# Performance work log

Measured on AMD Instinct MI355X. Metric: run time of the kernel, lower is better.

The kernel has to match this reference:

```python
import jax, jax.numpy as jnp
import numpy as np
from jax import lax

N = 4096
D = 256          # dim_hidden
DU = 1024        # dim_uni
G = 2000         # num_genes
E = 4            # num_experts
K = 1            # top-k
H = 4            # attention heads
HD = D // H      # head dim = 64
MAP = 64         # fourier mapping_size


def _ln(x, g, b, eps=1e-5):
    m = jnp.mean(x, axis=-1, keepdims=True)
    v = jnp.var(x, axis=-1, keepdims=True)
    return (x - m) * lax.rsqrt(v + eps) * g + b


def setup_inputs() -> dict:
    key = jax.random.key(0)
    ks = jax.random.split(key, 32)
    s = 0.02
    inp = {
        "vis": jax.random.normal(ks[0], (N, DU), jnp.float32),
        "pos": jax.random.uniform(ks[1], (N, 3), jnp.float32),
        "grad": jax.random.uniform(ks[2], (N, 1), jnp.float32),
        # FourierEncoding buffer: randn(3, 64) * scale(10)
        "B_fourier": jax.random.normal(ks[3], (3, MAP), jnp.float32) * 10.0,
        # img_enc
        "W_img": jax.random.normal(ks[4], (DU, D), jnp.float32) * s,
        "b_img": jnp.zeros((D,), jnp.float32),
        # pos_enc linear: Linear(128, 256)
        "W_pos": jax.random.normal(ks[5], (2 * MAP, D), jnp.float32) * s,
        "b_pos": jnp.zeros((D,), jnp.float32),
        # MultiheadAttention projections
        "Wq": jax.random.normal(ks[6], (D, D), jnp.float32) * s,
        "bq": jnp.zeros((D,), jnp.float32),
        "Wk": jax.random.normal(ks[7], (D, D), jnp.float32) * s,
        "bk": jnp.zeros((D,), jnp.float32),
        "Wv": jax.random.normal(ks[8], (D, D), jnp.float32) * s,
        "bv": jnp.zeros((D,), jnp.float32),
        "Wo": jax.random.normal(ks[9], (D, D), jnp.float32) * s,
        "bo": jnp.zeros((D,), jnp.float32),
        "ln1_g": jnp.ones((D,), jnp.float32),
        "ln1_b": jnp.zeros((D,), jnp.float32),
        # MoE router: Linear(D+1, E)
        "W_router": jax.random.normal(ks[10], (D + 1, E), jnp.float32) * s,
        "b_router": jnp.zeros((E,), jnp.float32),
        # experts: stacked [E, ...] FFN weights
        "W1e": jax.random.normal(ks[11], (E, D, 4 * D), jnp.float32) * s,
        "b1e": jnp.zeros((E, 4 * D), jnp.float32),
        "W2e": jax.random.normal(ks[12], (E, 4 * D, D), jnp.float32) * s,
        "b2e": jnp.zeros((E, D), jnp.float32),
        # gene decoder
        "Wg1": jax.random.normal(ks[13], (D, D), jnp.float32) * s,
        "bg1": jnp.zeros((D,), jnp.float32),
        "lng_g": jnp.ones((D,), jnp.float32),
        "lng_b": jnp.zeros((D,), jnp.float32),
        "Wg2": jax.random.normal(ks[14], (D, 2 * G), jnp.float32) * s,
        "bg2": jnp.zeros((2 * G,), jnp.float32),
        # func head
        "Wf1": jax.random.normal(ks[15], (D, 64), jnp.float32) * s,
        "bf1": jnp.zeros((64,), jnp.float32),
        "Wf2": jax.random.normal(ks[16], (64, 1), jnp.float32) * s,
        "bf2": jnp.zeros((1,), jnp.float32),
    }
    return inp


def reference(vis, pos, grad, B_fourier, W_img, b_img, W_pos, b_pos,
              Wq, bq, Wk, bk, Wv, bv, Wo, bo, ln1_g, ln1_b,
              W_router, b_router, W1e, b1e, W2e, b2e,
              Wg1, bg1, lng_g, lng_b, Wg2, bg2, Wf1, bf1, Wf2, bf2):
    # --- encoders ---
    x_proj = (2.0 * np.pi) * (pos @ B_fourier)                 # [N, 64]
    fourier = jnp.concatenate([jnp.sin(x_proj), jnp.cos(x_proj)], axis=-1)  # [N,128]
    z = vis @ W_img + b_img + fourier @ W_pos + b_pos          # [N, D]

    # --- spatial context attention (batch=1 full self-attention) ---
    q = (z @ Wq + bq).reshape(N, H, HD)
    k = (z @ Wk + bk).reshape(N, H, HD)
    v = (z @ Wv + bv).reshape(N, H, HD)
    scores = jnp.einsum('nhd,mhd->hnm', q, k) / np.sqrt(HD)    # [H, N, N]
    attn = jax.nn.softmax(scores, axis=-1)
    ctx = jnp.einsum('hnm,mhd->nhd', attn, v).reshape(N, D)
    attn_out = ctx @ Wo + bo
    z = _ln(z + attn_out, ln1_g, ln1_b)

    # --- sparse MoE (top-1 routing, gated dense expert combine) ---
    router_in = jnp.concatenate([z, grad], axis=-1)            # [N, D+1]
    logits = router_in @ W_router + b_router                   # [N, E]
    probs = jax.nn.softmax(logits, axis=-1)
    topk_p, topk_i = lax.top_k(probs, K)                       # [N, K]
    gate = jnp.sum(jax.nn.one_hot(topk_i, E, dtype=z.dtype) * topk_p[..., None], axis=1)  # [N, E]
    h = jax.nn.gelu(jnp.einsum('nd,edf->nef', z, W1e) + b1e, approximate=False)  # [N,E,4D]
    y = jnp.einsum('nef,efd->ned', h, W2e) + b2e               # [N, E, D]
    z = z + jnp.einsum('ne,ned->nd', gate, y)

    # --- gene decoder ---
    d = jax.nn.gelu(_ln(z @ Wg1 + bg1, lng_g, lng_b), approximate=False)
    preds = (d @ Wg2 + bg2).reshape(N, G, 2)
    mu = jax.nn.softplus(preds[:, :, 0])
    theta = jax.nn.softplus(preds[:, :, 1]) + 1e-6

    # --- functional head ---
    g = jax.nn.sigmoid(jax.nn.gelu(z @ Wf1 + bf1, approximate=False) @ Wf2 + bf2)
    return mu, theta, g
```

## Files before the change

kernel.cpp:

```cpp
#include <hip/hip_runtime.h>
#include <math.h>

#define NTOK 4096
#define DMODEL 256
#define G_GENES 2000

typedef _Float16 f16;
typedef _Float16 f16x8 __attribute__((ext_vector_type(8)));
typedef float f32x4 __attribute__((ext_vector_type(4)));

__device__ __forceinline__ float gelu_exact(float x) {
    return 0.5f * x * (1.0f + erff(x * 0.70710678118654752f));
}
__device__ __forceinline__ float softplus_fast(float x) {
    return fmaxf(x, 0.0f) + __logf(1.0f + __expf(-fabsf(x)));
}

__global__ __launch_bounds__(256) void encin_k(const float* __restrict__ vis,
                                               const float* __restrict__ pos,
                                               const float* __restrict__ B,
                                               f16* __restrict__ Abig) {
    int n = blockIdx.x, t = threadIdx.x;
    float4 v = *(const float4*)(vis + (size_t)n * 1024 + t * 4);
    union { ushort4 u; f16 h[4]; } o;
    o.h[0] = (f16)v.x; o.h[1] = (f16)v.y; o.h[2] = (f16)v.z; o.h[3] = (f16)v.w;
    *(ushort4*)(Abig + (size_t)n * 1152 + t * 4) = o.u;
    if (t < 64) {
        float xp = 6.283185307179586f *
                   (pos[n * 3 + 0] * B[t] + pos[n * 3 + 1] * B[64 + t] + pos[n * 3 + 2] * B[128 + t]);
        Abig[(size_t)n * 1152 + 1024 + t] = (f16)sinf(xp);
        Abig[(size_t)n * 1152 + 1088 + t] = (f16)cosf(xp);
    }
}

struct TD { const float* s; f16* d; int R, C; int ldo; };
struct TDs { TD t[17]; int pre[18]; };
__global__ __launch_bounds__(256) void tconv_k(TDs ds) {
    int bid = blockIdx.x;
    int ti = 0;
#pragma unroll
    for (int i = 0; i < 17; i++)
        if (bid >= ds.pre[i + 1]) ti = i + 1;
    TD td = ds.t[ti];
    int local = bid - ds.pre[ti];
    int yt = td.C >> 5;
    int r0 = (local / yt) << 5;
    int c0 = (local % yt) << 5;
    __shared__ float tile[32][33];
    int tx = threadIdx.x & 31, ty = threadIdx.x >> 5;
#pragma unroll
    for (int i = 0; i < 32; i += 8)
        tile[ty + i][tx] = td.s[(size_t)(r0 + ty + i) * td.C + c0 + tx];
    __syncthreads();
#pragma unroll
    for (int i = 0; i < 32; i += 8)
        td.d[(size_t)(c0 + ty + i) * td.ldo + r0 + tx] = (f16)tile[tx][ty + i];
}

__global__ __launch_bounds__(256) void tconvh_k(const f16* __restrict__ src, int ldin,
                                                f16* __restrict__ dst, int ldo) {
    __shared__ f16 tile[32][33];
    int r0 = blockIdx.x * 32, c0 = blockIdx.y * 32;
    int tx = threadIdx.x & 31, ty = threadIdx.x >> 5;
#pragma unroll
    for (int i = 0; i < 32; i += 8)
        tile[ty + i][tx] = src[(size_t)(r0 + ty + i) * ldin + c0 + tx];
    __syncthreads();
#pragma unroll
    for (int i = 0; i < 32; i += 8)
        dst[(size_t)(c0 + ty + i) * ldo + r0 + tx] = tile[tx][ty + i];
}

__global__ __launch_bounds__(256) void setup_k(const float* b_img, const float* b_pos,
                                               const float* bq, const float* bk, const float* bv,
                                               const float* bg1, const float* bf1,
                                               float* benc, float* biasqkv, float* bgf) {
    int t = threadIdx.x;
    benc[t] = b_img[t] + b_pos[t];
    biasqkv[t] = bq[t];
    biasqkv[256 + t] = bk[t];
    biasqkv[512 + t] = bv[t];
    bgf[t] = bg1[t];
    if (t < 64) bgf[256 + t] = bf1[t];
}

#define EPI_F32 0
#define EPI_DUAL 1
#define EPI_F16 2
#define EPI_GELU_F16 3
#define EPI_GENE 4
#define EPI_MOESC 5
#define EPI_GF 6

template <int MTN, int EPI, int MODE>
__global__ __launch_bounds__(256) void bgemm_k(
    const f16* __restrict__ A, int lda,
    const f16* __restrict__ B, int ldb,
    const float* __restrict__ bias,
    float* __restrict__ Cf, f16* __restrict__ Ch, int ldc,
    int Ncols, int K,
    size_t eB, size_t eBias,
    const int* __restrict__ gidx, const int* __restrict__ temap,
    const float* __restrict__ z2, const float* __restrict__ gval,
    float* __restrict__ outMu, float* __restrict__ outTheta) {
    constexpr int BN = MTN * 32;
    __shared__ __align__(16) char smem[(128 + BN) * 72 * 2];
    f16 (*As)[72] = (f16(*)[72])smem;
    f16 (*Bs)[72] = (f16(*)[72])(smem + (size_t)128 * 72 * 2);

    const int tid = threadIdx.x;
    const int m0 = blockIdx.x * 128;
    const int n0 = blockIdx.y * BN;
    const int w = tid >> 6, lane = tid & 63;
    const int wr = w >> 1, wc = w & 1;
    const int ln = lane & 15, lg = lane >> 4;
    const int sr = tid >> 3;
    const int sc = (tid & 7) * 8;

    if (MODE == 1 || MODE == 2) {
        int e = temap[blockIdx.x];
        B += (size_t)e * eB;
        if (bias) bias += (size_t)e * eBias;
    }

    int grows[4];
#pragma unroll
    for (int i = 0; i < 4; i++) {
        int r = m0 + sr + i * 32;
        if (MODE == 1) {
            int g = gidx[r];
            grows[i] = (g < 0) ? 0 : g;
        } else {
            grows[i] = r;
        }
    }

    f32x4 acc[4][MTN];
    f32x4 zf = {0.f, 0.f, 0.f, 0.f};
#pragma unroll
    for (int i = 0; i < 4; i++)
#pragma unroll
        for (int j = 0; j < MTN; j++) acc[i][j] = zf;

    for (int k0 = 0; k0 < K; k0 += 64) {
#pragma unroll
        for (int i = 0; i < 4; i++) {
            uint4 v = *(const uint4*)(A + (size_t)grows[i] * lda + k0 + sc);
            int r = sr + i * 32;
            *(uint2*)&As[r][sc] = make_uint2(v.x, v.y);
            *(uint2*)&As[r][sc + 4] = make_uint2(v.z, v.w);
        }
#pragma unroll
        for (int i = 0; i < MTN; i++) {
            int r = sr + i * 32;
            uint4 v = make_uint4(0, 0, 0, 0);
            if (n0 + r < Ncols) v = *(const uint4*)(B + (size_t)(n0 + r) * ldb + k0 + sc);
            *(uint2*)&Bs[r][sc] = make_uint2(v.x, v.y);
            *(uint2*)&Bs[r][sc + 4] = make_uint2(v.z, v.w);
        }
        __syncthreads();
#pragma unroll
        for (int ks = 0; ks < 64; ks += 32) {
            f16x8 a[4], b[MTN];
#pragma unroll
            for (int t = 0; t < 4; t++) {
                const f16* p = &As[wr * 64 + t * 16 + ln][ks + lg * 8];
                union { f16x8 f; uint2 u[2]; } tmp;
                tmp.u[0] = *(const uint2*)p;
                tmp.u[1] = *(const uint2*)(p + 4);
                a[t] = tmp.f;
            }
#pragma unroll
            for (int t = 0; t < MTN; t++) {
                const f16* p = &Bs[wc * (MTN * 16) + t * 16 + ln][ks + lg * 8];
                union { f16x8 f; uint2 u[2]; } tmp;
                tmp.u[0] = *(const uint2*)p;
                tmp.u[1] = *(const uint2*)(p + 4);
                b[t] = tmp.f;
            }
#pragma unroll
            for (int tm = 0; tm < 4; tm++)
#pragma unroll
                for (int tn = 0; tn < MTN; tn++)
                    acc[tm][tn] = __builtin_amdgcn_mfma_f32_16x16x32_f16(a[tm], b[tn], acc[tm][tn], 0, 0, 0);
        }
        __syncthreads();
    }

    if (EPI == EPI_GENE) {
        float bval[MTN];
#pragma unroll
        for (int tn = 0; tn < MTN; tn++) {
            int col = n0 + wc * (MTN * 16) + tn * 16 + ln;
            bval[tn] = (col < Ncols) ? bias[col] : 0.0f;
        }
        float* Cs = (float*)smem;
        const int rrow = tid >> 3;
        const int rseg = tid & 7;
#pragma unroll
        for (int tm = 0; tm < 4; tm++) {
            __syncthreads();
#pragma unroll
            for (int tn = 0; tn < MTN; tn++) {
                int lc = wc * (MTN * 16) + tn * 16 + ln;
#pragma unroll
                for (int i = 0; i < 4; i++) {
                    int lr = wr * 16 + lg * 4 + i;
                    Cs[lr * 132 + lc] = acc[tm][tn][i] + bval[tn];
                }
            }
            __syncthreads();
            int grow = m0 + ((rrow >> 4) * 64) + tm * 16 + (rrow & 15);
            const float* cr = &Cs[rrow * 132 + rseg * 16];
            float mu[8], th[8];
#pragma unroll
            for (int g = 0; g < 8; g++) {
                mu[g] = softplus_fast(cr[2 * g]);
                th[g] = softplus_fast(cr[2 * g + 1]) + 1e-6f;
            }
            int gbase = (n0 + rseg * 16) >> 1;
            float* mp = outMu + (size_t)grow * G_GENES + gbase;
            float* tp = outTheta + (size_t)grow * G_GENES + gbase;
            if (gbase + 8 <= G_GENES) {
                *(float4*)mp = make_float4(mu[0], mu[1], mu[2], mu[3]);
                *(float4*)(mp + 4) = make_float4(mu[4], mu[5], mu[6], mu[7]);
                *(float4*)tp = make_float4(th[0], th[1], th[2], th[3]);
                *(float4*)(tp + 4) = make_float4(th[4], th[5], th[6], th[7]);
            } else {
#pragma unroll
                for (int g = 0; g < 8; g++)
                    if (gbase + g < G_GENES) { mp[g] = mu[g]; tp[g] = th[g]; }
            }
        }
        return;
    }

#pragma unroll
    for (int tm = 0; tm < 4; tm++) {
#pragma unroll
        for (int tn = 0; tn < MTN; tn++) {
            int col = n0 + wc * (MTN * 16) + tn * 16 + ln;
            if (col >= Ncols) continue;
#pragma unroll
            for (int i = 0; i < 4; i++) {
                int row = m0 + wr * 64 + tm * 16 + lg * 4 + i;
                float v = acc[tm][tn][i];
                if (EPI == EPI_MOESC) {
                    int tok = gidx[row];
                    if (tok < 0) continue;
                    v += bias[col];
                    size_t oi = (size_t)tok * ldc + col;
                    Ch[oi] = (f16)(z2[oi] + gval[tok] * v);
                    continue;
                }
                if (EPI == EPI_GF) {
                    v += bias[col];
                    if (col < 256) Cf[(size_t)row * 256 + col] = v;
                    else Ch[(size_t)row * 64 + (col - 256)] = (f16)gelu_exact(v);
                    continue;
                }
                size_t idx = (size_t)row * ldc + col;
                if (EPI == EPI_F32) {
                    if (bias) v += bias[col];
                    Cf[idx] = v;
                } else if (EPI == EPI_DUAL) {
                    v += bias[col];
                    Cf[idx] = v;
                    Ch[idx] = (f16)v;
                } else if (EPI == EPI_F16) {
                    v += bias[col];
                    Ch[idx] = (f16)v;
                } else if (EPI == EPI_GELU_F16) {
                    v += bias[col];
                    Ch[idx] = (f16)gelu_exact(v);
                }
            }
        }
    }
}

__global__ __launch_bounds__(256) void flash_k(const f16* __restrict__ qkv,
                                               const f16* __restrict__ Vt,
                                               f16* __restrict__ Opart16,
                                               float2* __restrict__ mlpart) {
    __shared__ f16 Ks[64][72];
    __shared__ f16 Vts[64][72];
    __shared__ f16 Ps[4][16][72];
    const int tid = threadIdx.x;
    const int w = tid >> 6, lane = tid & 63;
    const int ln = lane & 15, quad = lane >> 4;
    const int q0 = blockIdx.x * 64;
    const int hq = blockIdx.y * 64;
    const int kt0 = blockIdx.z * 8;

    f16x8 qfrag[2];
    {
        const f16* qp = qkv + (size_t)(q0 + w * 16 + ln) * 768 + hq + quad * 8;
        union { f16x8 f; uint4 u; } t0, t1;
        t0.u = *(const uint4*)qp;
        t1.u = *(const uint4*)(qp + 32);
        qfrag[0] = t0.f; qfrag[1] = t1.f;
    }

    const int srow = tid >> 2;
    const int scol = (tid & 3) * 16;

    float m_run[4], l_run[4];
    f32x4 Oacc[4];
#pragma unroll
    for (int i = 0; i < 4; i++) {
        m_run[i] = -1e30f; l_run[i] = 0.0f;
        Oacc[i] = (f32x4){0.f, 0.f, 0.f, 0.f};
    }

    uint4 kreg[2], vreg[2];
    {
        const f16* kp = qkv + (size_t)(kt0 * 64 + srow) * 768 + 256 + hq + scol;
        const f16* vp = Vt + (size_t)(hq + srow) * 4096 + kt0 * 64 + scol;
        kreg[0] = *(const uint4*)kp; kreg[1] = *(const uint4*)(kp + 8);
        vreg[0] = *(const uint4*)vp; vreg[1] = *(const uint4*)(vp + 8);
    }

    for (int kt = kt0; kt < kt0 + 8; kt++) {
        __syncthreads();
        *(uint4*)&Ks[srow][scol] = kreg[0];
        *(uint4*)&Ks[srow][scol + 8] = kreg[1];
        *(uint4*)&Vts[srow][scol] = vreg[0];
        *(uint4*)&Vts[srow][scol + 8] = vreg[1];
        __syncthreads();
        if (kt + 1 < kt0 + 8) {
            const f16* kp = qkv + (size_t)((kt + 1) * 64 + srow) * 768 + 256 + hq + scol;
            const f16* vp = Vt + (size_t)(hq + srow) * 4096 + (kt + 1) * 64 + scol;
            kreg[0] = *(const uint4*)kp; kreg[1] = *(const uint4*)(kp + 8);
            vreg[0] = *(const uint4*)vp; vreg[1] = *(const uint4*)(vp + 8);
        }

        f32x4 accS[4];
#pragma unroll
        for (int nt = 0; nt < 4; nt++) {
            union { f16x8 f; uint4 u; } b0, b1;
            b0.u = *(const uint4*)&Ks[nt * 16 + ln][quad * 8];
            b1.u = *(const uint4*)&Ks[nt * 16 + ln][32 + quad * 8];
            f32x4 a = {0.f, 0.f, 0.f, 0.f};
            a = __builtin_amdgcn_mfma_f32_16x16x32_f16(qfrag[0], b0.f, a, 0, 0, 0);
            a = __builtin_amdgcn_mfma_f32_16x16x32_f16(qfrag[1], b1.f, a, 0, 0, 0);
            accS[nt] = a;
        }
#pragma unroll
        for (int nt = 0; nt < 4; nt++)
#pragma unroll
            for (int i = 0; i < 4; i++) accS[nt][i] *= 0.125f;

        float mnew[4], alpha[4], rs[4];
#pragma unroll
        for (int i = 0; i < 4; i++) {
            float mx = fmaxf(fmaxf(accS[0][i], accS[1][i]), fmaxf(accS[2][i], accS[3][i]));
            mx = fmaxf(mx, __shfl_xor(mx, 1));
            mx = fmaxf(mx, __shfl_xor(mx, 2));
            mx = fmaxf(mx, __shfl_xor(mx, 4));
            mx = fmaxf(mx, __shfl_xor(mx, 8));
            mnew[i] = fmaxf(m_run[i], mx);
            rs[i] = 0.0f;
        }
#pragma unroll
        for (int nt = 0; nt < 4; nt++)
#pragma unroll
            for (int i = 0; i < 4; i++) {
                float p = __expf(accS[nt][i] - mnew[i]);
                accS[nt][i] = p;
                rs[i] += p;
            }
#pragma unroll
        for (int i = 0; i < 4; i++) {
            float s = rs[i];
            s += __shfl_xor(s, 1);
            s += __shfl_xor(s, 2);
            s += __shfl_xor(s, 4);
            s += __shfl_xor(s, 8);
            alpha[i] = __expf(m_run[i] - mnew[i]);
            l_run[i] = l_run[i] * alpha[i] + s;
            m_run[i] = mnew[i];
        }
#pragma unroll
        for (int dt = 0; dt < 4; dt++)
#pragma unroll
            for (int i = 0; i < 4; i++) Oacc[dt][i] *= alpha[i];

#pragma unroll
        for (int nt = 0; nt < 4; nt++)
#pragma unroll
            for (int i = 0; i < 4; i++)
                Ps[w][quad * 4 + i][nt * 16 + ln] = (f16)accS[nt][i];

        union { f16x8 f; uint4 u; } pf0, pf1;
        pf0.u = *(const uint4*)&Ps[w][ln][quad * 8];
        pf1.u = *(const uint4*)&Ps[w][ln][32 + quad * 8];
#pragma unroll
        for (int dt = 0; dt < 4; dt++) {
            union { f16x8 f; uint4 u; } b0, b1;
            b0.u = *(const uint4*)&Vts[dt * 16 + ln][quad * 8];
            b1.u = *(const uint4*)&Vts[dt * 16 + ln][32 + quad * 8];
            Oacc[dt] = __builtin_amdgcn_mfma_f32_16x16x32_f16(pf0.f, b0.f, Oacc[dt], 0, 0, 0);
            Oacc[dt] = __builtin_amdgcn_mfma_f32_16x16x32_f16(pf1.f, b1.f, Oacc[dt], 0, 0, 0);
        }
    }

    const int slot = blockIdx.x * 4 + blockIdx.y;
    f16* op = Opart16 + ((((size_t)blockIdx.z * 256 + slot) * 4 + w) * 64 + lane) * 16;
    union { uint4 u; f16 h[8]; } pk0, pk1;
#pragma unroll
    for (int dt = 0; dt < 2; dt++)
#pragma unroll
        for (int i = 0; i < 4; i++) pk0.h[dt * 4 + i] = (f16)Oacc[dt][i];
#pragma unroll
    for (int dt = 2; dt < 4; dt++)
#pragma unroll
        for (int i = 0; i < 4; i++) pk1.h[(dt - 2) * 4 + i] = (f16)Oacc[dt][i];
    *(uint4*)op = pk0.u;
    *(uint4*)(op + 8) = pk1.u;
    if (ln == 0) {
#pragma unroll
        for (int i = 0; i < 4; i++)
            mlpart[(size_t)(blockIdx.z * 4 + blockIdx.y) * NTOK + q0 + w * 16 + quad * 4 + i] =
                make_float2(m_run[i], l_run[i]);
    }
}

__global__ __launch_bounds__(256) void fcomb_k(const f16* __restrict__ Opart16,
                                               const float2* __restrict__ mlpart,
                                               f16* __restrict__ ctxbf) {
    const int slot = blockIdx.x;
    const int w = threadIdx.x >> 6, lane = threadIdx.x & 63;
    const int bx = slot >> 2, h = slot & 3;
    const int quad = lane >> 4, ln = lane & 15;
    const int nbase = bx * 64 + w * 16 + quad * 4;

    float2 ml[8][4];
    float mmax[4] = {-1e30f, -1e30f, -1e30f, -1e30f};
#pragma unroll
    for (int s = 0; s < 8; s++)
#pragma unroll
        for (int i = 0; i < 4; i++) {
            ml[s][i] = mlpart[(size_t)(s * 4 + h) * NTOK + nbase + i];
            mmax[i] = fmaxf(mmax[i], ml[s][i].x);
        }
    float L[4] = {0.f, 0.f, 0.f, 0.f};
    float wgt[8][4];
#pragma unroll
    for (int s = 0; s < 8; s++)
#pragma unroll
        for (int i = 0; i < 4; i++) {
            wgt[s][i] = __expf(ml[s][i].x - mmax[i]);
            L[i] += wgt[s][i] * ml[s][i].y;
        }

    float acc[16];
#pragma unroll
    for (int j = 0; j < 16; j++) acc[j] = 0.f;
#pragma unroll
    for (int s = 0; s < 8; s++) {
        const f16* op = Opart16 + ((((size_t)s * 256 + slot) * 4 + w) * 64 + lane) * 16;
        union { uint4 u; f16 h[8]; } p0, p1;
        p0.u = *(const uint4*)op;
        p1.u = *(const uint4*)(op + 8);
#pragma unroll
        for (int dt = 0; dt < 2; dt++)
#pragma unroll
            for (int i = 0; i < 4; i++) acc[dt * 4 + i] += wgt[s][i] * (float)p0.h[dt * 4 + i];
#pragma unroll
        for (int dt = 2; dt < 4; dt++)
#pragma unroll
            for (int i = 0; i < 4; i++) acc[dt * 4 + i] += wgt[s][i] * (float)p1.h[(dt - 2) * 4 + i];
    }
    float inv[4];
#pragma unroll
    for (int i = 0; i < 4; i++) inv[i] = 1.0f / L[i];
#pragma unroll
    for (int dt = 0; dt < 4; dt++)
#pragma unroll
        for (int i = 0; i < 4; i++)
            ctxbf[(size_t)(nbase + i) * 256 + h * 64 + dt * 16 + ln] = (f16)(acc[dt * 4 + i] * inv[i]);
}

template <int DO_ROUTER>
__global__ __launch_bounds__(256) void ln_k(const float* __restrict__ X,
                                            const float* __restrict__ R,
                                            const float* __restrict__ gam,
                                            const float* __restrict__ bet,
                                            float* __restrict__ Of, f16* __restrict__ Oh, int doGelu,
                                            const float* __restrict__ grad,
                                            const float* __restrict__ Wr,
                                            const float* __restrict__ br,
                                            int* __restrict__ eid, float* __restrict__ gval) {
    __shared__ float sm[4];
    __shared__ float smr[16];
    int n = blockIdx.x, c = threadIdx.x;
    float x = X[(size_t)n * DMODEL + c];
    if (R) x += R[(size_t)n * DMODEL + c];
    float s = x;
    for (int off = 32; off; off >>= 1) s += __shfl_down(s, off);
    if ((c & 63) == 0) sm[c >> 6] = s;
    __syncthreads();
    float mean = (sm[0] + sm[1] + sm[2] + sm[3]) * (1.0f / DMODEL);
    float d = x - mean;
    float s2 = d * d;
    for (int off = 32; off; off >>= 1) s2 += __shfl_down(s2, off);
    __syncthreads();
    if ((c & 63) == 0) sm[c >> 6] = s2;
    __syncthreads();
    float var = (sm[0] + sm[1] + sm[2] + sm[3]) * (1.0f / DMODEL);
    float y = d * rsqrtf(var + 1e-5f) * gam[c] + bet[c];
    if (doGelu) y = gelu_exact(y);
    size_t idx = (size_t)n * DMODEL + c;
    if (Of) Of[idx] = y;
    if (Oh) Oh[idx] = (f16)y;

    if (DO_ROUTER) {
        float p0 = y * Wr[c * 4 + 0], p1 = y * Wr[c * 4 + 1];
        float p2 = y * Wr[c * 4 + 2], p3 = y * Wr[c * 4 + 3];
        for (int off = 32; off; off >>= 1) {
            p0 += __shfl_down(p0, off);
            p1 += __shfl_down(p1, off);
            p2 += __shfl_down(p2, off);
            p3 += __shfl_down(p3, off);
        }
        int wv = c >> 6;
        if ((c & 63) == 0) {
            smr[wv * 4 + 0] = p0; smr[wv * 4 + 1] = p1;
            smr[wv * 4 + 2] = p2; smr[wv * 4 + 3] = p3;
        }
        __syncthreads();
        if (c == 0) {
            float gv = grad[n];
            float l[4];
#pragma unroll
            for (int e = 0; e < 4; e++)
                l[e] = smr[e] + smr[4 + e] + smr[8 + e] + smr[12 + e] + gv * Wr[256 * 4 + e] + br[e];
            float mx = fmaxf(fmaxf(l[0], l[1]), fmaxf(l[2], l[3]));
            float ex[4], ssum = 0;
#pragma unroll
            for (int e = 0; e < 4; e++) { ex[e] = __expf(l[e] - mx); ssum += ex[e]; }
            int am = 0;
            float best = l[0];
#pragma unroll
            for (int e = 1; e < 4; e++)
                if (l[e] > best) { best = l[e]; am = e; }
            eid[n] = am;
            gval[n] = ex[am] / ssum;
        }
    }
}

__global__ __launch_bounds__(256) void compact_k(const int* __restrict__ eid,
                                                 int* __restrict__ gidx,
                                                 int* __restrict__ temap) {
    __shared__ int cnt[4], poff[4], cur[4];
    int t = threadIdx.x;
    if (t < 4) cnt[t] = 0;
    __syncthreads();
    for (int it = 0; it < 16; it++)
        atomicAdd(&cnt[eid[it * 256 + t]], 1);
    __syncthreads();
    if (t == 0) {
        int o = 0;
        for (int e = 0; e < 4; e++) {
            poff[e] = o;
            cur[e] = o;
            o += (cnt[e] + 127) & ~127;
        }
    }
    __syncthreads();
    if (t < 36) {
        int e = 0;
        for (int x = 0; x < 4; x++) {
            int seg0 = poff[x] >> 7;
            int seg1 = (poff[x] + ((cnt[x] + 127) & ~127)) >> 7;
            if (t >= seg0 && t < seg1) e = x;
        }
        temap[t] = e;
    }
    for (int i = t; i < 4608; i += 256) gidx[i] = -1;
    __syncthreads();
    for (int it = 0; it < 16; it++) {
        int n = it * 256 + t;
        int slot = atomicAdd(&cur[eid[n]], 1);
        gidx[slot] = n;
    }
}

__global__ __launch_bounds__(256) void ghead_k(const f16* __restrict__ f,
                                               const float* __restrict__ Wf2,
                                               const float* __restrict__ bf2,
                                               float* __restrict__ out) {
    int n = blockIdx.x * 256 + threadIdx.x;
    float s = bf2[0];
#pragma unroll
    for (int c = 0; c < 8; c++) {
        union { uint4 u; f16 h[8]; } t;
        t.u = *(const uint4*)(f + (size_t)n * 64 + c * 8);
#pragma unroll
        for (int j = 0; j < 8; j++) s = fmaf((float)t.h[j], Wf2[c * 8 + j], s);
    }
    out[n] = 1.0f / (1.0f + expf(-s));
}

extern "C" void kernel_launch(void* const* d_in, const int* in_sizes, int n_in,
                              void* d_out, int out_size, void* d_ws, size_t ws_size,
                              hipStream_t stream) {
    const float* vis   = (const float*)d_in[0];
    const float* pos   = (const float*)d_in[1];
    const float* grad  = (const float*)d_in[2];
    const float* Bf    = (const float*)d_in[3];
    const float* W_img = (const float*)d_in[4];
    const float* b_img = (const float*)d_in[5];
    const float* W_pos = (const float*)d_in[6];
    const float* b_pos = (const float*)d_in[7];
    const float* Wq = (const float*)d_in[8];  const float* bq = (const float*)d_in[9];
    const float* Wk = (const float*)d_in[10]; const float* bk = (const float*)d_in[11];
    const float* Wv = (const float*)d_in[12]; const float* bv = (const float*)d_in[13];
    const float* Wo = (const float*)d_in[14]; const float* bo = (const float*)d_in[15];
    const float* ln1g = (const float*)d_in[16]; const float* ln1b = (const float*)d_in[17];
    const float* Wr = (const float*)d_in[18]; const float* br = (const float*)d_in[19];
    const float* W1e = (const float*)d_in[20]; const float* b1e = (const float*)d_in[21];
    const float* W2e = (const float*)d_in[22]; const float* b2e = (const float*)d_in[23];
    const float* Wg1 = (const float*)d_in[24]; const float* bg1 = (const float*)d_in[25];
    const float* lngg = (const float*)d_in[26]; const float* lngb = (const float*)d_in[27];
    const float* Wg2 = (const float*)d_in[28]; const float* bg2 = (const float*)d_in[29];
    const float* Wf1 = (const float*)d_in[30]; const float* bf1 = (const float*)d_in[31];
    const float* Wf2 = (const float*)d_in[32]; const float* bf2 = (const float*)d_in[33];

    float* out = (float*)d_out;
    float* outMu = out;
    float* outTh = out + (size_t)NTOK * G_GENES;
    float* outG  = out + (size_t)2 * NTOK * G_GENES;

    char* base = (char*)d_ws;
    size_t off = 0;
    auto A8 = [&](size_t bytes) { char* p = base + off; off += (bytes + 255) & ~(size_t)255; return p; };

    char* reg1 = A8(16 * 1024 * 1024);
    f16* Abig    = (f16*)reg1;
    f16* Opart16 = (f16*)reg1;
    char* reg2 = A8(20 * 1024 * 1024);
    f16* qkvbf = (f16*)reg2;
    f16* hh    = (f16*)(reg2 + 8 * 1024 * 1024);

    f16* WtEnc = (f16*)A8((size_t)256 * 1152 * 2);
    f16* Wqkvt = (f16*)A8((size_t)768 * 256 * 2);
    f16* Wot   = (f16*)A8((size_t)256 * 256 * 2);
    f16* W1t   = (f16*)A8((size_t)4 * 1024 * 256 * 2);
    f16* W2t   = (f16*)A8((size_t)4 * 256 * 1024 * 2);
    f16* Wgft  = (f16*)A8((size_t)320 * 256 * 2);
    f16* Wg2t  = (f16*)A8((size_t)4000 * 256 * 2);
    f16* Vt    = (f16*)A8((size_t)256 * NTOK * 2);
    float2* mlpart = (float2*)A8((size_t)32 * NTOK * 8);
    float* benc    = (float*)A8(256 * 4);
    float* biasqkv = (float*)A8(768 * 4);
    float* bgf     = (float*)A8(320 * 4);
    float* z    = (float*)A8((size_t)NTOK * DMODEL * 4);
    float* z2   = (float*)A8((size_t)NTOK * DMODEL * 4);
    float* attn = (float*)A8((size_t)NTOK * DMODEL * 4);
    float* tbuf = (float*)A8((size_t)NTOK * DMODEL * 4);
    f16* zbf    = (f16*)A8((size_t)NTOK * DMODEL * 2);
    f16* z2bf   = (f16*)A8((size_t)NTOK * DMODEL * 2);
    f16* z3bf   = (f16*)A8((size_t)NTOK * DMODEL * 2);
    f16* ctxbf  = (f16*)A8((size_t)NTOK * DMODEL * 2);
    f16* dbufbf = (f16*)A8((size_t)NTOK * DMODEL * 2);
    f16* fbf    = (f16*)A8((size_t)NTOK * 64 * 2);
    int* eidb   = (int*)A8(NTOK * 4);
    float* gval = (float*)A8(NTOK * 4);
    int* gidx   = (int*)A8(4608 * 4);
    int* temap  = (int*)A8(64 * 4);

    dim3 blk(256);

    TDs td;
    int nd = 0, pre = 0;
    auto addT = [&](const float* s, f16* d, int R, int C, int ldo) {
        td.t[nd] = TD{s, d, R, C, ldo};
        td.pre[nd] = pre;
        pre += (R >> 5) * (C >> 5);
        nd++;
    };
    addT(W_img, WtEnc, 1024, 256, 1152);
    addT(W_pos, WtEnc + 1024, 128, 256, 1152);
    addT(Wq, Wqkvt, 256, 256, 256);
    addT(Wk, Wqkvt + 256 * 256, 256, 256, 256);
    addT(Wv, Wqkvt + 512 * 256, 256, 256, 256);
    addT(Wo, Wot, 256, 256, 256);
    for (int e = 0; e < 4; e++) addT(W1e + (size_t)e * 262144, W1t + (size_t)e * 262144, 256, 1024, 256);
    for (int e = 0; e < 4; e++) addT(W2e + (size_t)e * 262144, W2t + (size_t)e * 262144, 1024, 256, 1024);
    addT(Wg1, Wgft, 256, 256, 256);
    addT(Wf1, Wgft + 256 * 256, 256, 64, 256);
    addT(Wg2, Wg2t, 256, 4000, 256);
    td.pre[nd] = pre;
    tconv_k<<<pre, blk, 0, stream>>>(td);
    setup_k<<<1, blk, 0, stream>>>(b_img, b_pos, bq, bk, bv, bg1, bf1, benc, biasqkv, bgf);

    encin_k<<<NTOK, blk, 0, stream>>>(vis, pos, Bf, Abig);
    bgemm_k<1, EPI_DUAL, 0><<<dim3(32, 8, 1), blk, 0, stream>>>(
        Abig, 1152, WtEnc, 1152, benc, z, zbf, 256, 256, 1152,
        0, 0, nullptr, nullptr, nullptr, nullptr, nullptr, nullptr);

    bgemm_k<2, EPI_F16, 0><<<dim3(32, 12, 1), blk, 0, stream>>>(
        zbf, 256, Wqkvt, 256, biasqkv, nullptr, qkvbf, 768, 768, 256,
        0, 0, nullptr, nullptr, nullptr, nullptr, nullptr, nullptr);
    tconvh_k<<<dim3(128, 8, 1), blk, 0, stream>>>(qkvbf + 512, 768, Vt, 4096);

    flash_k<<<dim3(64, 4, 8), blk, 0, stream>>>(qkvbf, Vt, Opart16, mlpart);
    fcomb_k<<<256, blk, 0, stream>>>(Opart16, mlpart, ctxbf);
    bgemm_k<1, EPI_F32, 0><<<dim3(32, 8, 1), blk, 0, stream>>>(
        ctxbf, 256, Wot, 256, bo, attn, nullptr, 256, 256, 256,
        0, 0, nullptr, nullptr, nullptr, nullptr, nullptr, nullptr);
    ln_k<1><<<NTOK, blk, 0, stream>>>(z, attn, ln1g, ln1b, z2, z2bf, 0, grad, Wr, br, eidb, gval);

    compact_k<<<1, blk, 0, stream>>>(eidb, gidx, temap);
    bgemm_k<4, EPI_GELU_F16, 1><<<dim3(36, 8, 1), blk, 0, stream>>>(
        z2bf, 256, W1t, 256, b1e, nullptr, hh, 1024, 1024, 256,
        262144, 1024, gidx, temap, nullptr, nullptr, nullptr, nullptr);
    bgemm_k<2, EPI_MOESC, 2><<<dim3(36, 4, 1), blk, 0, stream>>>(
        hh, 1024, W2t, 1024, b2e, nullptr, z3bf, 256, 256, 1024,
        262144, 256, gidx, temap, z2, gval, nullptr, nullptr);

    bgemm_k<1, EPI_GF, 0><<<dim3(32, 10, 1), blk, 0, stream>>>(
        z3bf, 256, Wgft, 256, bgf, tbuf, fbf, 256, 320, 256,
        0, 0, nullptr, nullptr, nullptr, nullptr, nullptr, nullptr);
    ln_k<0><<<NTOK, blk, 0, stream>>>(tbuf, nullptr, lngg, lngb, nullptr, dbufbf, 1,
                                      nullptr, nullptr, nullptr, nullptr, nullptr);
    bgemm_k<4, EPI_GENE, 0><<<dim3(32, 32, 1), blk, 0, stream>>>(
        dbufbf, 256, Wg2t, 256, bg2, nullptr, nullptr, 4000, 4000, 256,
        0, 0, nullptr, nullptr, nullptr, nullptr, outMu, outTh);

    ghead_k<<<NTOK / 256, blk, 0, stream>>>(fbf, Wf2, bf2, outG);
}
```

Baseline: 479.2 us.

## Transpose flash attention MFMA, double-buffer K/V, halve KV splits, retile MoE down-proj

The flash-attention kernel swaps the MFMA operand order, computing S^T, so each lane holds a single query row. This turns the row max and sum into two cross-quad shuffles and lets P be rebuilt in registers via shuffles instead of a shared-memory round trip. K/V tiles are double-buffered in LDS with one barrier per tile, and each block covers 16 key tiles instead of 8, which halves the split-K partials that fcomb has to merge. fcomb now writes its output through LDS to get vectorized stores, and the MoE second GEMM changes its tile template from 2 to 1 with twice as many column blocks. Fewer splits reduce parallelism in flash_k (1024 blocks instead of 2048) in exchange for less combine traffic.

```diff
diff --git a/kernel.cpp b/kernel.cpp
--- a/kernel.cpp
+++ b/kernel.cpp
@@ -6,6 +6,7 @@
 #define G_GENES 2000
 
 typedef _Float16 f16;
+typedef _Float16 f16x2 __attribute__((ext_vector_type(2)));
 typedef _Float16 f16x8 __attribute__((ext_vector_type(8)));
 typedef float f32x4 __attribute__((ext_vector_type(4)));
 
@@ -14,6 +15,11 @@
 }
 __device__ __forceinline__ float softplus_fast(float x) {
     return fmaxf(x, 0.0f) + __logf(1.0f + __expf(-fabsf(x)));
+}
+__device__ __forceinline__ unsigned pkf16(float a, float b) {
+    union { f16x2 h; unsigned u; } t;
+    t.h = (f16x2){(f16)a, (f16)b};
+    return t.u;
 }
 
 __global__ __launch_bounds__(256) void encin_k(const float* __restrict__ vis,
@@ -283,15 +289,14 @@
                                                const f16* __restrict__ Vt,
                                                f16* __restrict__ Opart16,
                                                float2* __restrict__ mlpart) {
-    __shared__ f16 Ks[64][72];
-    __shared__ f16 Vts[64][72];
-    __shared__ f16 Ps[4][16][72];
+    __shared__ f16 Kb[2][64][72];
+    __shared__ f16 Vb[2][64][72];
     const int tid = threadIdx.x;
     const int w = tid >> 6, lane = tid & 63;
     const int ln = lane & 15, quad = lane >> 4;
     const int q0 = blockIdx.x * 64;
     const int hq = blockIdx.y * 64;
-    const int kt0 = blockIdx.z * 8;
+    const int kt0 = blockIdx.z * 16;
 
     f16x8 qfrag[2];
     {
@@ -305,104 +310,106 @@
     const int srow = tid >> 2;
     const int scol = (tid & 3) * 16;
 
-    float m_run[4], l_run[4];
-    f32x4 Oacc[4];
-#pragma unroll
-    for (int i = 0; i < 4; i++) {
-        m_run[i] = -1e30f; l_run[i] = 0.0f;
-        Oacc[i] = (f32x4){0.f, 0.f, 0.f, 0.f};
-    }
-
-    uint4 kreg[2], vreg[2];
-    {
-        const f16* kp = qkv + (size_t)(kt0 * 64 + srow) * 768 + 256 + hq + scol;
-        const f16* vp = Vt + (size_t)(hq + srow) * 4096 + kt0 * 64 + scol;
-        kreg[0] = *(const uint4*)kp; kreg[1] = *(const uint4*)(kp + 8);
-        vreg[0] = *(const uint4*)vp; vreg[1] = *(const uint4*)(vp + 8);
-    }
-
-    for (int kt = kt0; kt < kt0 + 8; kt++) {
+    float m_run = -1e30f, l_run = 0.0f;
+    f32x4 accO[4];
+#pragma unroll
+    for (int i = 0; i < 4; i++) accO[i] = (f32x4){0.f, 0.f, 0.f, 0.f};
+
+    uint4 kA[2], vA[2], kB[2], vB[2];
+    auto loadKV = [&](int kt, uint4* kr, uint4* vr) {
+        const f16* kp = qkv + (size_t)(kt * 64 + srow) * 768 + 256 + hq + scol;
+        const f16* vp = Vt + (size_t)(hq + srow) * 4096 + kt * 64 + scol;
+        kr[0] = *(const uint4*)kp; kr[1] = *(const uint4*)(kp + 8);
+        vr[0] = *(const uint4*)vp; vr[1] = *(const uint4*)(vp + 8);
+    };
+    auto stage = [&](int b, const uint4* kr, const uint4* vr) {
+        *(uint4*)&Kb[b][srow][scol] = kr[0];
+        *(uint4*)&Kb[b][srow][scol + 8] = kr[1];
+        *(uint4*)&Vb[b][srow][scol] = vr[0];
+        *(uint4*)&Vb[b][srow][scol + 8] = vr[1];
+    };
+
+    auto computeTile = [&](int b) {
+        f32x4 accS[4];
+#pragma unroll
+        for (int nt = 0; nt < 4; nt++) {
+            union { f16x8 f; uint4 u; } a0, a1;
+            a0.u = *(const uint4*)&Kb[b][nt * 16 + ln][quad * 8];
+            a1.u = *(const uint4*)&Kb[b][nt * 16 + ln][32 + quad * 8];
+            f32x4 a = {0.f, 0.f, 0.f, 0.f};
+            a = __builtin_amdgcn_mfma_f32_16x16x32_f16(a0.f, qfrag[0], a, 0, 0, 0);
+            a = __builtin_amdgcn_mfma_f32_16x16x32_f16(a1.f, qfrag[1], a, 0, 0, 0);
+            accS[nt] = a;
+        }
+        float mx = -1e30f;
+#pragma unroll
+        for (int nt = 0; nt < 4; nt++)
+#pragma unroll
+            for (int i = 0; i < 4; i++) {
+                accS[nt][i] *= 0.125f;
+                mx = fmaxf(mx, accS[nt][i]);
+            }
+        mx = fmaxf(mx, __shfl_xor(mx, 16));
+        mx = fmaxf(mx, __shfl_xor(mx, 32));
+        float mnew = fmaxf(m_run, mx);
+        float rs = 0.0f;
+#pragma unroll
+        for (int nt = 0; nt < 4; nt++)
+#pragma unroll
+            for (int i = 0; i < 4; i++) {
+                float p = __expf(accS[nt][i] - mnew);
+                accS[nt][i] = p;
+                rs += p;
+            }
+        rs += __shfl_xor(rs, 16);
+        rs += __shfl_xor(rs, 32);
+        float alpha = __expf(m_run - mnew);
+        l_run = l_run * alpha + rs;
+        m_run = mnew;
+#pragma unroll
+        for (int dt = 0; dt < 4; dt++)
+#pragma unroll
+            for (int i = 0; i < 4; i++) accO[dt][i] *= alpha;
+
+#pragma unroll
+        for (int c = 0; c < 2; c++) {
+            unsigned p0x = pkf16(accS[2 * c][0], accS[2 * c][1]);
+            unsigned p0y = pkf16(accS[2 * c][2], accS[2 * c][3]);
+            unsigned p1x = pkf16(accS[2 * c + 1][0], accS[2 * c + 1][1]);
+            unsigned p1y = pkf16(accS[2 * c + 1][2], accS[2 * c + 1][3]);
+            unsigned x16_0x = __shfl_xor((int)p0x, 16), x16_0y = __shfl_xor((int)p0y, 16);
+            unsigned x32_0x = __shfl_xor((int)p0x, 32), x32_0y = __shfl_xor((int)p0y, 32);
+            unsigned x48_0x = __shfl_xor((int)p0x, 48), x48_0y = __shfl_xor((int)p0y, 48);
+            unsigned x16_1x = __shfl_xor((int)p1x, 16), x16_1y = __shfl_xor((int)p1y, 16);
+            unsigned x32_1x = __shfl_xor((int)p1x, 32), x32_1y = __shfl_xor((int)p1y, 32);
+            unsigned x48_1x = __shfl_xor((int)p1x, 48), x48_1y = __shfl_xor((int)p1y, 48);
+            union { f16x8 f; unsigned u[4]; } pf;
+            pf.u[0] = quad == 0 ? p0x : quad == 1 ? x48_0x : quad == 2 ? x32_1x : x16_1x;
+            pf.u[1] = quad == 0 ? p0y : quad == 1 ? x48_0y : quad == 2 ? x32_1y : x16_1y;
+            pf.u[2] = quad == 0 ? x16_0x : quad == 1 ? x32_0x : quad == 2 ? x48_1x : p1x;
+            pf.u[3] = quad == 0 ? x16_0y : quad == 1 ? x32_0y : quad == 2 ? x48_1y : p1y;
+#pragma unroll
+            for (int dt = 0; dt < 4; dt++) {
+                union { f16x8 f; uint4 u; } vf;
+                vf.u = *(const uint4*)&Vb[b][dt * 16 + ln][c * 32 + quad * 8];
+                accO[dt] = __builtin_amdgcn_mfma_f32_16x16x32_f16(vf.f, pf.f, accO[dt], 0, 0, 0);
+            }
+        }
+    };
+
+    loadKV(kt0, kA, vA);
+    stage(0, kA, vA);
+    loadKV(kt0 + 1, kB, vB);
+    __syncthreads();
+    for (int t = 0; t < 16; t += 2) {
+        computeTile(0);
+        stage(1, kB, vB);
+        if (t + 2 < 16) loadKV(kt0 + t + 2, kA, vA);
         __syncthreads();
-        *(uint4*)&Ks[srow][scol] = kreg[0];
-        *(uint4*)&Ks[srow][scol + 8] = kreg[1];
-        *(uint4*)&Vts[srow][scol] = vreg[0];
-        *(uint4*)&Vts[srow][scol + 8] = vreg[1];
+        computeTile(1);
+        if (t + 2 < 16) stage(0, kA, vA);
+        if (t + 3 < 16) loadKV(kt0 + t + 3, kB, vB);
         __syncthreads();
-        if (kt + 1 < kt0 + 8) {
-            const f16* kp = qkv + (size_t)((kt + 1) * 64 + srow) * 768 + 256 + hq + scol;
-            const f16* vp = Vt + (size_t)(hq + srow) * 4096 + (kt + 1) * 64 + scol;
-            kreg[0] = *(const uint4*)kp; kreg[1] = *(const uint4*)(kp + 8);
-            vreg[0] = *(const uint4*)vp; vreg[1] = *(const uint4*)(vp + 8);
-        }
-
-        f32x4 accS[4];
-#pragma unroll
-        for (int nt = 0; nt < 4; nt++) {
-            union { f16x8 f; uint4 u; } b0, b1;
-            b0.u = *(const uint4*)&Ks[nt * 16 + ln][quad * 8];
-            b1.u = *(const uint4*)&Ks[nt * 16 + ln][32 + quad * 8];
-            f32x4 a = {0.f, 0.f, 0.f, 0.f};
-            a = __builtin_amdgcn_mfma_f32_16x16x32_f16(qfrag[0], b0.f, a, 0, 0, 0);
-            a = __builtin_amdgcn_mfma_f32_16x16x32_f16(qfrag[1], b1.f, a, 0, 0, 0);
-            accS[nt] = a;
-        }
-#pragma unroll
-        for (int nt = 0; nt < 4; nt++)
-#pragma unroll
-            for (int i = 0; i < 4; i++) accS[nt][i] *= 0.125f;
-
-        float mnew[4], alpha[4], rs[4];
-#pragma unroll
-        for (int i = 0; i < 4; i++) {
-            float mx = fmaxf(fmaxf(accS[0][i], accS[1][i]), fmaxf(accS[2][i], accS[3][i]));
-            mx = fmaxf(mx, __shfl_xor(mx, 1));
-            mx = fmaxf(mx, __shfl_xor(mx, 2));
-            mx = fmaxf(mx, __shfl_xor(mx, 4));
-            mx = fmaxf(mx, __shfl_xor(mx, 8));
-            mnew[i] = fmaxf(m_run[i], mx);
-            rs[i] = 0.0f;
-        }
-#pragma unroll
-        for (int nt = 0; nt < 4; nt++)
-#pragma unroll
-            for (int i = 0; i < 4; i++) {
-                float p = __expf(accS[nt][i] - mnew[i]);
-                accS[nt][i] = p;
-                rs[i] += p;
-            }
-#pragma unroll
-        for (int i = 0; i < 4; i++) {
-            float s = rs[i];
-            s += __shfl_xor(s, 1);
-            s += __shfl_xor(s, 2);
-            s += __shfl_xor(s, 4);
-            s += __shfl_xor(s, 8);
-            alpha[i] = __expf(m_run[i] - mnew[i]);
-            l_run[i] = l_run[i] * alpha[i] + s;
-            m_run[i] = mnew[i];
-        }
-#pragma unroll
-        for (int dt = 0; dt < 4; dt++)
-#pragma unroll
-            for (int i = 0; i < 4; i++) Oacc[dt][i] *= alpha[i];
-
-#pragma unroll
-        for (int nt = 0; nt < 4; nt++)
-#pragma unroll
-            for (int i = 0; i < 4; i++)
-                Ps[w][quad * 4 + i][nt * 16 + ln] = (f16)accS[nt][i];
-
-        union { f16x8 f; uint4 u; } pf0, pf1;
-        pf0.u = *(const uint4*)&Ps[w][ln][quad * 8];
-        pf1.u = *(const uint4*)&Ps[w][ln][32 + quad * 8];
-#pragma unroll
-        for (int dt = 0; dt < 4; dt++) {
-            union { f16x8 f; uint4 u; } b0, b1;
-            b0.u = *(const uint4*)&Vts[dt * 16 + ln][quad * 8];
-            b1.u = *(const uint4*)&Vts[dt * 16 + ln][32 + quad * 8];
-            Oacc[dt] = __builtin_amdgcn_mfma_f32_16x16x32_f16(pf0.f, b0.f, Oacc[dt], 0, 0, 0);
-            Oacc[dt] = __builtin_amdgcn_mfma_f32_16x16x32_f16(pf1.f, b1.f, Oacc[dt], 0, 0, 0);
-        }
     }
 
     const int slot = blockIdx.x * 4 + blockIdx.y;
@@ -411,75 +418,68 @@
 #pragma unroll
     for (int dt = 0; dt < 2; dt++)
 #pragma unroll
-        for (int i = 0; i < 4; i++) pk0.h[dt * 4 + i] = (f16)Oacc[dt][i];
+        for (int i = 0; i < 4; i++) pk0.h[dt * 4 + i] = (f16)accO[dt][i];
 #pragma unroll
     for (int dt = 2; dt < 4; dt++)
 #pragma unroll
-        for (int i = 0; i < 4; i++) pk1.h[(dt - 2) * 4 + i] = (f16)Oacc[dt][i];
+        for (int i = 0; i < 4; i++) pk1.h[(dt - 2) * 4 + i] = (f16)accO[dt][i];
     *(uint4*)op = pk0.u;
     *(uint4*)(op + 8) = pk1.u;
-    if (ln == 0) {
-#pragma unroll
-        for (int i = 0; i < 4; i++)
-            mlpart[(size_t)(blockIdx.z * 4 + blockIdx.y) * NTOK + q0 + w * 16 + quad * 4 + i] =
-                make_float2(m_run[i], l_run[i]);
-    }
+    if (quad == 0)
+        mlpart[(size_t)(blockIdx.z * 4 + blockIdx.y) * NTOK + q0 + w * 16 + ln] =
+            make_float2(m_run, l_run);
 }
 
 __global__ __launch_bounds__(256) void fcomb_k(const f16* __restrict__ Opart16,
                                                const float2* __restrict__ mlpart,
                                                f16* __restrict__ ctxbf) {
+    __shared__ f16 Os[4][16][72];
     const int slot = blockIdx.x;
     const int w = threadIdx.x >> 6, lane = threadIdx.x & 63;
     const int bx = slot >> 2, h = slot & 3;
     const int quad = lane >> 4, ln = lane & 15;
-    const int nbase = bx * 64 + w * 16 + quad * 4;
-
-    float2 ml[8][4];
-    float mmax[4] = {-1e30f, -1e30f, -1e30f, -1e30f};
-#pragma unroll
-    for (int s = 0; s < 8; s++)
-#pragma unroll
-        for (int i = 0; i < 4; i++) {
-            ml[s][i] = mlpart[(size_t)(s * 4 + h) * NTOK + nbase + i];
-            mmax[i] = fmaxf(mmax[i], ml[s][i].x);
-        }
-    float L[4] = {0.f, 0.f, 0.f, 0.f};
-    float wgt[8][4];
-#pragma unroll
-    for (int s = 0; s < 8; s++)
-#pragma unroll
-        for (int i = 0; i < 4; i++) {
-            wgt[s][i] = __expf(ml[s][i].x - mmax[i]);
-            L[i] += wgt[s][i] * ml[s][i].y;
-        }
-
+    const int q = bx * 64 + w * 16 + ln;
+
+    float2 ml[4];
+    float mmax = -1e30f;
+#pragma unroll
+    for (int s = 0; s < 4; s++) {
+        ml[s] = mlpart[(size_t)(s * 4 + h) * NTOK + q];
+        mmax = fmaxf(mmax, ml[s].x);
+    }
+    float L = 0.0f, wgt[4];
+#pragma unroll
+    for (int s = 0; s < 4; s++) {
+        wgt[s] = __expf(ml[s].x - mmax);
+        L += wgt[s] * ml[s].y;
+    }
     float acc[16];
 #pragma unroll
     for (int j = 0; j < 16; j++) acc[j] = 0.f;
 #pragma unroll
-    for (int s = 0; s < 8; s++) {
+    for (int s = 0; s < 4; s++) {
         const f16* op = Opart16 + ((((size_t)s * 256 + slot) * 4 + w) * 64 + lane) * 16;
-        union { uint4 u; f16 h[8]; } p0, p1;
+        union { uint4 u; f16 hh[8]; } p0, p1;
         p0.u = *(const uint4*)op;
         p1.u = *(const uint4*)(op + 8);
 #pragma unroll
-        for (int dt = 0; dt < 2; dt++)
-#pragma unroll
-            for (int i = 0; i < 4; i++) acc[dt * 4 + i] += wgt[s][i] * (float)p0.h[dt * 4 + i];
-#pragma unroll
-        for (int dt = 2; dt < 4; dt++)
-#pragma unroll
-            for (int i = 0; i < 4; i++) acc[dt * 4 + i] += wgt[s][i] * (float)p1.h[(dt - 2) * 4 + i];
-    }
-    float inv[4];
-#pragma unroll
-    for (int i = 0; i < 4; i++) inv[i] = 1.0f / L[i];
+        for (int j = 0; j < 8; j++) {
+            acc[j] += wgt[s] * (float)p0.hh[j];
+            acc[8 + j] += wgt[s] * (float)p1.hh[j];
+        }
+    }
+    float inv = 1.0f / L;
 #pragma unroll
     for (int dt = 0; dt < 4; dt++)
 #pragma unroll
         for (int i = 0; i < 4; i++)
-            ctxbf[(size_t)(nbase + i) * 256 + h * 64 + dt * 16 + ln] = (f16)(acc[dt * 4 + i] * inv[i]);
+            Os[w][ln][dt * 16 + quad * 4 + i] = (f16)(acc[dt * 4 + i] * inv);
+    union { uint4 u; f16 hh[8]; } o0, o1;
+    o0.u = *(const uint4*)&Os[w][ln][quad * 16];
+    o1.u = *(const uint4*)&Os[w][ln][quad * 16 + 8];
+    f16* cp = ctxbf + (size_t)q * 256 + h * 64 + quad * 16;
+    *(uint4*)cp = o0.u;
+    *(uint4*)(cp + 8) = o1.u;
 }
 
 template <int DO_ROUTER>
@@ -653,7 +653,7 @@
     f16* Wgft  = (f16*)A8((size_t)320 * 256 * 2);
     f16* Wg2t  = (f16*)A8((size_t)4000 * 256 * 2);
     f16* Vt    = (f16*)A8((size_t)256 * NTOK * 2);
-    float2* mlpart = (float2*)A8((size_t)32 * NTOK * 8);
+    float2* mlpart = (float2*)A8((size_t)16 * NTOK * 8);
     float* benc    = (float*)A8(256 * 4);
     float* biasqkv = (float*)A8(768 * 4);
     float* bgf     = (float*)A8(320 * 4);
@@ -707,7 +707,7 @@
         0, 0, nullptr, nullptr, nullptr, nullptr, nullptr, nullptr);
     tconvh_k<<<dim3(128, 8, 1), blk, 0, stream>>>(qkvbf + 512, 768, Vt, 4096);
 
-    flash_k<<<dim3(64, 4, 8), blk, 0, stream>>>(qkvbf, Vt, Opart16, mlpart);
+    flash_k<<<dim3(64, 4, 4), blk, 0, stream>>>(qkvbf, Vt, Opart16, mlpart);
     fcomb_k<<<256, blk, 0, stream>>>(Opart16, mlpart, ctxbf);
     bgemm_k<1, EPI_F32, 0><<<dim3(32, 8, 1), blk, 0, stream>>>(
         ctxbf, 256, Wot, 256, bo, attn, nullptr, 256, 256, 256,
@@ -718,7 +718,7 @@
     bgemm_k<4, EPI_GELU_F16, 1><<<dim3(36, 8, 1), blk, 0, stream>>>(
         z2bf, 256, W1t, 256, b1e, nullptr, hh, 1024, 1024, 256,
         262144, 1024, gidx, temap, nullptr, nullptr, nullptr, nullptr);
-    bgemm_k<2, EPI_MOESC, 2><<<dim3(36, 4, 1), blk, 0, stream>>>(
+    bgemm_k<1, EPI_MOESC, 2><<<dim3(36, 8, 1), blk, 0, stream>>>(
         hh, 1024, W2t, 1024, b2e, nullptr, z3bf, 256, 256, 1024,
         262144, 256, gidx, temap, z2, gval, nullptr, nullptr);
 
```

Result: faster. 437.1 us (-8.8%).
